# Kernel tuning notes

Measured on AMD Instinct MI355X. Metric: run time of the kernel, lower is better.

The kernel has to match this reference:

```python
import jax, jax.numpy as jnp
import numpy as np

N, D, E = 40000, 128, 640000
ALPHA = 0.1   # GCNII alpha
BETA = 1.0    # GCN2Conv theta=None => beta = 1.0
BN_EPS = 1e-5


def setup_inputs() -> dict:
    key = jax.random.key(0)
    ks = jax.random.split(key, 5)
    x = jax.random.normal(ks[0], (N, D), jnp.float32)
    x_orig = jax.random.normal(ks[1], (N, D), jnp.float32)
    edge_index = jax.random.randint(ks[2], (2, E), 0, N, dtype=jnp.int64)
    edge_weights = jax.random.uniform(ks[3], (E,), jnp.float32)
    W = jax.random.normal(ks[4], (D, D), jnp.float32) / np.sqrt(D).astype(np.float32)
    gamma = jnp.ones((D,), jnp.float32)
    beta = jnp.zeros((D,), jnp.float32)
    return dict(x=x, x_orig=x_orig, edge_index=edge_index,
                edge_weights=edge_weights, W=W, gamma=gamma, beta=beta)


def _gcn_norm(edge_index, edge_weight, num_nodes):
    # PyG gcn_norm: add self loops (weight 1), symmetric D^{-1/2} A D^{-1/2}
    loop = jnp.arange(num_nodes, dtype=edge_index.dtype)
    row = jnp.concatenate([edge_index[0], loop])   # source
    col = jnp.concatenate([edge_index[1], loop])   # target
    ew = jnp.concatenate([edge_weight, jnp.ones((num_nodes,), edge_weight.dtype)])
    deg = jax.ops.segment_sum(ew, col, num_segments=num_nodes)
    dis = jnp.where(deg > 0, jax.lax.rsqrt(deg), 0.0)
    norm = dis[row] * ew * dis[col]
    return row, col, norm


def reference(x, x_orig, edge_index, edge_weights, W, gamma, beta):
    n = x.shape[0]
    row, col, norm = _gcn_norm(edge_index, edge_weights, n)
    # sparse neighbor aggregation: gather x[row], scale, scatter-add to col
    agg = jax.ops.segment_sum(norm[:, None] * x[row], col, num_segments=n)
    # GCNII initial-residual blend; theta=None => out = blended @ W (beta=1)
    h = ((1.0 - ALPHA) * agg + ALPHA * x_orig) @ W
    h = jax.nn.relu(h)
    # BatchNorm1d (training mode: batch statistics, biased variance)
    mean = h.mean(axis=0)
    var = h.var(axis=0)
    h = (h - mean) * jax.lax.rsqrt(var + BN_EPS) * gamma + beta
    return h
```

## Files before the change

### kernel.cpp

```cpp
#include <hip/hip_runtime.h>

#define NN 40000
#define DD 128
#define EE 640000

__global__ __launch_bounds__(256) void k_init(int* __restrict__ cnt,
                                              float* __restrict__ sums) {
    int i = blockIdx.x * 256 + threadIdx.x;
    if (i < NN) cnt[i] = 0;
    if (i < 256) sums[i] = 0.0f;
}

__global__ __launch_bounds__(256) void k_rank(const int* __restrict__ ei,
                                              int* __restrict__ cnt,
                                              int* __restrict__ rank) {
    int e = blockIdx.x * 256 + threadIdx.x;
    int c = ei[EE + e];
    rank[e] = atomicAdd(&cnt[c], 1);
}

#define SCAN_CH 40
__global__ __launch_bounds__(1024) void k_scan(const int* __restrict__ cnt,
                                               int* __restrict__ off) {
    __shared__ int sm[1024];
    int t = threadIdx.x;
    int base = t * SCAN_CH;
    int s = 0;
    if (base < NN) {
#pragma unroll
        for (int i = 0; i < SCAN_CH; ++i) s += cnt[base + i];
    }
    sm[t] = s;
    __syncthreads();
    for (int d = 1; d < 1024; d <<= 1) {
        int v = (t >= d) ? sm[t - d] : 0;
        __syncthreads();
        sm[t] += v;
        __syncthreads();
    }
    if (base < NN) {
        int run = sm[t] - s;
#pragma unroll
        for (int i = 0; i < SCAN_CH; ++i) {
            off[base + i] = run;
            run += cnt[base + i];
        }
    }
    if (t == 1023) off[NN] = sm[1023];
}

__global__ __launch_bounds__(256) void k_permute(const int* __restrict__ ei,
                                                 const float* __restrict__ ew,
                                                 const int* __restrict__ rank,
                                                 const int* __restrict__ off,
                                                 int2* __restrict__ srn) {
    int e = blockIdx.x * 256 + threadIdx.x;
    int r = ei[e], c = ei[EE + e];
    int pos = off[c] + rank[e];
    srn[pos] = make_int2(r, __float_as_int(ew[e]));
}

__global__ __launch_bounds__(256) void k_degdis(const int* __restrict__ off,
                                                const int2* __restrict__ srn,
                                                float* __restrict__ dis) {
    int gid = blockIdx.x * 256 + threadIdx.x;
    int node = gid >> 6;
    int lane = gid & 63;
    int s = off[node], e = off[node + 1];
    float v = 0.0f;
    for (int p = s + lane; p < e; p += 64) v += __int_as_float(srn[p].y);
#pragma unroll
    for (int m = 1; m < 64; m <<= 1) v += __shfl_xor(v, m);
    if (lane == 0) dis[node] = rsqrtf(1.0f + v);
}

__global__ __launch_bounds__(256) void k_gather(const int* __restrict__ off,
                                                const int2* __restrict__ srn,
                                                const float* __restrict__ x,
                                                const float* __restrict__ xorig,
                                                const float* __restrict__ dis,
                                                float* __restrict__ blend) {
    int gid = blockIdx.x * 256 + threadIdx.x;
    int wave = gid >> 6;
    int lane = gid & 63;
    int half = lane >> 5;
    int l32  = lane & 31;
    int node = wave * 2 + half;
    int srcb = half << 5;
    const float4* x4 = (const float4*)x;

    float dc = dis[node];
    float4 sv = x4[(size_t)node * 32 + l32];
    float4 acc0 = {sv.x * dc, sv.y * dc, sv.z * dc, sv.w * dc};
    float4 acc1 = {0, 0, 0, 0}, acc2 = {0, 0, 0, 0}, acc3 = {0, 0, 0, 0};

    int p = off[node], eend = off[node + 1];
    while (__any(p < eend)) {
        int ee = p + l32;
        bool act = ee < eend;
        int2 rv = act ? srn[ee] : make_int2(0, 0);
        float dl = act ? dis[rv.x] : 0.0f;
        float nm = __int_as_float(rv.y) * dl;
        int nb = eend - p;
        nb = nb < 0 ? 0 : (nb > 32 ? 32 : nb);
        int j = 0;
        for (; j + 4 <= nb; j += 4) {
            int r0 = __shfl(rv.x, srcb + j);
            int r1 = __shfl(rv.x, srcb + j + 1);
            int r2 = __shfl(rv.x, srcb + j + 2);
            int r3 = __shfl(rv.x, srcb + j + 3);
            float n0 = __shfl(nm, srcb + j);
            float n1 = __shfl(nm, srcb + j + 1);
            float n2 = __shfl(nm, srcb + j + 2);
            float n3 = __shfl(nm, srcb + j + 3);
            float4 v0 = x4[(size_t)r0 * 32 + l32];
            float4 v1 = x4[(size_t)r1 * 32 + l32];
            float4 v2 = x4[(size_t)r2 * 32 + l32];
            float4 v3 = x4[(size_t)r3 * 32 + l32];
            acc0.x = fmaf(n0, v0.x, acc0.x); acc0.y = fmaf(n0, v0.y, acc0.y);
            acc0.z = fmaf(n0, v0.z, acc0.z); acc0.w = fmaf(n0, v0.w, acc0.w);
            acc1.x = fmaf(n1, v1.x, acc1.x); acc1.y = fmaf(n1, v1.y, acc1.y);
            acc1.z = fmaf(n1, v1.z, acc1.z); acc1.w = fmaf(n1, v1.w, acc1.w);
            acc2.x = fmaf(n2, v2.x, acc2.x); acc2.y = fmaf(n2, v2.y, acc2.y);
            acc2.z = fmaf(n2, v2.z, acc2.z); acc2.w = fmaf(n2, v2.w, acc2.w);
            acc3.x = fmaf(n3, v3.x, acc3.x); acc3.y = fmaf(n3, v3.y, acc3.y);
            acc3.z = fmaf(n3, v3.z, acc3.z); acc3.w = fmaf(n3, v3.w, acc3.w);
        }
        for (; j < nb; ++j) {
            int rr = __shfl(rv.x, srcb + j);
            float nn = __shfl(nm, srcb + j);
            float4 v = x4[(size_t)rr * 32 + l32];
            acc0.x = fmaf(nn, v.x, acc0.x); acc0.y = fmaf(nn, v.y, acc0.y);
            acc0.z = fmaf(nn, v.z, acc0.z); acc0.w = fmaf(nn, v.w, acc0.w);
        }
        p += 32;
    }
    float4 xo = ((const float4*)xorig)[(size_t)node * 32 + l32];
    float4 bl;
    bl.x = 0.9f * (dc * (acc0.x + acc1.x + acc2.x + acc3.x)) + 0.1f * xo.x;
    bl.y = 0.9f * (dc * (acc0.y + acc1.y + acc2.y + acc3.y)) + 0.1f * xo.y;
    bl.z = 0.9f * (dc * (acc0.z + acc1.z + acc2.z + acc3.z)) + 0.1f * xo.z;
    bl.w = 0.9f * (dc * (acc0.w + acc1.w + acc2.w + acc3.w)) + 0.1f * xo.w;
    ((float4*)blend)[(size_t)node * 32 + l32] = bl;
}

__global__ __launch_bounds__(256) void k_matmul(const float* __restrict__ blend,
                                                const float* __restrict__ W,
                                                float* __restrict__ out) {
    int id = blockIdx.x;
    int rowblk, colhalf;
    if (id >= 624) { rowblk = 312; colhalf = id - 624; }
    else { rowblk = ((id >> 4) << 3) | (id & 7); colhalf = (id >> 3) & 1; }

    __shared__ float Wl[DD * 64];
    int t = threadIdx.x;
    int jb = colhalf << 6;
    {
#pragma unroll
        for (int i = 0; i < 8; ++i) {
            int idx = i * 256 + t;
            int k = idx >> 4, jq = idx & 15;
            *(float4*)&Wl[k * 64 + jq * 4] =
                *(const float4*)&W[(size_t)k * DD + jb + jq * 4];
        }
    }
    __syncthreads();

    int rg = t >> 3;
    int cg = t & 7;
    int row0 = rowblk * 128 + rg * 4;
    bool valid = (row0 + 3) < NN;
    size_t rr = valid ? (size_t)row0 : 0;
    int jc = cg * 8;

    float acc[4][8] = {};
    const float* ap = blend + rr * DD;

    for (int k0 = 0; k0 < DD; k0 += 4) {
        float in[4][4];
#pragma unroll
        for (int r = 0; r < 4; ++r) {
            float4 av = *(const float4*)(ap + r * DD + k0);
            in[r][0] = av.x; in[r][1] = av.y; in[r][2] = av.z; in[r][3] = av.w;
        }
#pragma unroll
        for (int kk = 0; kk < 4; ++kk) {
            float4 w0 = *(const float4*)&Wl[(k0 + kk) * 64 + jc];
            float4 w1 = *(const float4*)&Wl[(k0 + kk) * 64 + jc + 4];
#pragma unroll
            for (int r = 0; r < 4; ++r) {
                float a = in[r][kk];
                acc[r][0] = fmaf(a, w0.x, acc[r][0]);
                acc[r][1] = fmaf(a, w0.y, acc[r][1]);
                acc[r][2] = fmaf(a, w0.z, acc[r][2]);
                acc[r][3] = fmaf(a, w0.w, acc[r][3]);
                acc[r][4] = fmaf(a, w1.x, acc[r][4]);
                acc[r][5] = fmaf(a, w1.y, acc[r][5]);
                acc[r][6] = fmaf(a, w1.z, acc[r][6]);
                acc[r][7] = fmaf(a, w1.w, acc[r][7]);
            }
        }
    }
    if (valid) {
#pragma unroll
        for (int r = 0; r < 4; ++r) {
            float* orow = out + (rr + r) * DD + jb + jc;
            float4 v0 = {fmaxf(acc[r][0], 0.0f), fmaxf(acc[r][1], 0.0f),
                         fmaxf(acc[r][2], 0.0f), fmaxf(acc[r][3], 0.0f)};
            float4 v1 = {fmaxf(acc[r][4], 0.0f), fmaxf(acc[r][5], 0.0f),
                         fmaxf(acc[r][6], 0.0f), fmaxf(acc[r][7], 0.0f)};
            *(float4*)(orow) = v0;
            *(float4*)(orow + 4) = v1;
        }
    }
}

__global__ __launch_bounds__(256) void k_stats(const float* __restrict__ h,
                                               float* __restrict__ sums) {
    int t = threadIdx.x;
    int tid = blockIdx.x * 256 + t;
    int cg = t & 31;
    int row0 = tid >> 5;
    float4 s = {0, 0, 0, 0}, q = {0, 0, 0, 0};
    for (int r = row0; r < NN; r += 2048) {
        float4 v = *(const float4*)&h[(size_t)r * DD + cg * 4];
        s.x += v.x; s.y += v.y; s.z += v.z; s.w += v.w;
        q.x += v.x * v.x; q.y += v.y * v.y; q.z += v.z * v.z; q.w += v.w * v.w;
    }
    __shared__ float red[256][8];
    red[t][0] = s.x; red[t][1] = s.y; red[t][2] = s.z; red[t][3] = s.w;
    red[t][4] = q.x; red[t][5] = q.y; red[t][6] = q.z; red[t][7] = q.w;
    __syncthreads();
    if (t < 32) {
#pragma unroll
        for (int s8 = 1; s8 < 8; ++s8)
#pragma unroll
            for (int c = 0; c < 8; ++c) red[t][c] += red[t + 32 * s8][c];
        int j = t * 4;
        unsafeAtomicAdd(&sums[j + 0], red[t][0]);
        unsafeAtomicAdd(&sums[j + 1], red[t][1]);
        unsafeAtomicAdd(&sums[j + 2], red[t][2]);
        unsafeAtomicAdd(&sums[j + 3], red[t][3]);
        unsafeAtomicAdd(&sums[DD + j + 0], red[t][4]);
        unsafeAtomicAdd(&sums[DD + j + 1], red[t][5]);
        unsafeAtomicAdd(&sums[DD + j + 2], red[t][6]);
        unsafeAtomicAdd(&sums[DD + j + 3], red[t][7]);
    }
}

__global__ __launch_bounds__(256) void k_apply(float* __restrict__ h,
                                               const float* __restrict__ sums,
                                               const float* __restrict__ gamma,
                                               const float* __restrict__ beta) {
    int g = blockIdx.x * 256 + threadIdx.x;
    int i = g >> 5, q = g & 31;
    int j = q * 4;
    const float invN = 1.0f / (float)NN;
    float4 sm = *(const float4*)&sums[j];
    float4 sq = *(const float4*)&sums[DD + j];
    float4 gm = *(const float4*)&gamma[j];
    float4 bt = *(const float4*)&beta[j];
    float4 v = *(float4*)&h[(size_t)i * DD + j];
    float m0 = sm.x * invN, m1 = sm.y * invN, m2 = sm.z * invN, m3 = sm.w * invN;
    float i0 = rsqrtf(fmaxf(sq.x * invN - m0 * m0, 0.0f) + 1e-5f);
    float i1 = rsqrtf(fmaxf(sq.y * invN - m1 * m1, 0.0f) + 1e-5f);
    float i2 = rsqrtf(fmaxf(sq.z * invN - m2 * m2, 0.0f) + 1e-5f);
    float i3 = rsqrtf(fmaxf(sq.w * invN - m3 * m3, 0.0f) + 1e-5f);
    v.x = (v.x - m0) * i0 * gm.x + bt.x;
    v.y = (v.y - m1) * i1 * gm.y + bt.y;
    v.z = (v.z - m2) * i2 * gm.z + bt.z;
    v.w = (v.w - m3) * i3 * gm.w + bt.w;
    *(float4*)&h[(size_t)i * DD + j] = v;
}

extern "C" void kernel_launch(void* const* d_in, const int* in_sizes, int n_in,
                              void* d_out, int out_size, void* d_ws, size_t ws_size,
                              hipStream_t stream) {
    const float* x     = (const float*)d_in[0];
    const float* xorig = (const float*)d_in[1];
    const int*   ei    = (const int*)d_in[2];
    const float* ew    = (const float*)d_in[3];
    const float* W     = (const float*)d_in[4];
    const float* gamma = (const float*)d_in[5];
    const float* beta  = (const float*)d_in[6];
    float* out = (float*)d_out;

    float* ws    = (float*)d_ws;
    float* blend = ws;
    int2*  srn   = (int2*)(blend + (size_t)NN * DD);
    float* dis   = (float*)(srn + EE);
    float* sums  = dis + NN;
    int*   cnt   = (int*)(sums + 256);
    int*   off   = cnt + NN;
    int*   rank  = off + NN + 1;

    k_init   <<<160,   256, 0, stream>>>(cnt, sums);
    k_rank   <<<2500,  256, 0, stream>>>(ei, cnt, rank);
    k_scan   <<<1,    1024, 0, stream>>>(cnt, off);
    k_permute<<<2500,  256, 0, stream>>>(ei, ew, rank, off, srn);
    k_degdis <<<10000, 256, 0, stream>>>(off, srn, dis);
    k_gather <<<5000,  256, 0, stream>>>(off, srn, x, xorig, dis, blend);
    k_matmul <<<626,   256, 0, stream>>>(blend, W, out);
    k_stats  <<<256,   256, 0, stream>>>(out, sums);
    k_apply  <<<5000,  256, 0, stream>>>(out, sums, gamma, beta);
}
```

Before: 257.9 us.

## Fuse batchnorm statistics into matmul epilogue and unroll gather by eight

Each matmul block now accumulates per-column sum and sum-of-squares of its ReLU outputs, reduces them in shared memory and atomically adds them into the global sums. This removes the separate stats kernel and its full re-read of the output. The gather loop also now issues eight neighbour row loads per iteration instead of four, to keep more memory requests in flight. The costs are a larger shared-memory footprint in the matmul, more register pressure in the gather, and more atomics (626 blocks instead of 256).

```diff
diff --git a/kernel.cpp b/kernel.cpp
--- a/kernel.cpp
+++ b/kernel.cpp
@@ -91,8 +91,8 @@
 
     float dc = dis[node];
     float4 sv = x4[(size_t)node * 32 + l32];
-    float4 acc0 = {sv.x * dc, sv.y * dc, sv.z * dc, sv.w * dc};
-    float4 acc1 = {0, 0, 0, 0}, acc2 = {0, 0, 0, 0}, acc3 = {0, 0, 0, 0};
+    float4 a0 = {sv.x * dc, sv.y * dc, sv.z * dc, sv.w * dc};
+    float4 a1 = {0, 0, 0, 0}, a2 = {0, 0, 0, 0}, a3 = {0, 0, 0, 0};
 
     int p = off[node], eend = off[node + 1];
     while (__any(p < eend)) {
@@ -104,55 +104,55 @@
         int nb = eend - p;
         nb = nb < 0 ? 0 : (nb > 32 ? 32 : nb);
         int j = 0;
-        for (; j + 4 <= nb; j += 4) {
-            int r0 = __shfl(rv.x, srcb + j);
-            int r1 = __shfl(rv.x, srcb + j + 1);
-            int r2 = __shfl(rv.x, srcb + j + 2);
-            int r3 = __shfl(rv.x, srcb + j + 3);
-            float n0 = __shfl(nm, srcb + j);
-            float n1 = __shfl(nm, srcb + j + 1);
-            float n2 = __shfl(nm, srcb + j + 2);
-            float n3 = __shfl(nm, srcb + j + 3);
-            float4 v0 = x4[(size_t)r0 * 32 + l32];
-            float4 v1 = x4[(size_t)r1 * 32 + l32];
-            float4 v2 = x4[(size_t)r2 * 32 + l32];
-            float4 v3 = x4[(size_t)r3 * 32 + l32];
-            acc0.x = fmaf(n0, v0.x, acc0.x); acc0.y = fmaf(n0, v0.y, acc0.y);
-            acc0.z = fmaf(n0, v0.z, acc0.z); acc0.w = fmaf(n0, v0.w, acc0.w);
-            acc1.x = fmaf(n1, v1.x, acc1.x); acc1.y = fmaf(n1, v1.y, acc1.y);
-            acc1.z = fmaf(n1, v1.z, acc1.z); acc1.w = fmaf(n1, v1.w, acc1.w);
-            acc2.x = fmaf(n2, v2.x, acc2.x); acc2.y = fmaf(n2, v2.y, acc2.y);
-            acc2.z = fmaf(n2, v2.z, acc2.z); acc2.w = fmaf(n2, v2.w, acc2.w);
-            acc3.x = fmaf(n3, v3.x, acc3.x); acc3.y = fmaf(n3, v3.y, acc3.y);
-            acc3.z = fmaf(n3, v3.z, acc3.z); acc3.w = fmaf(n3, v3.w, acc3.w);
+        for (; j + 8 <= nb; j += 8) {
+            int r[8]; float n[8];
+#pragma unroll
+            for (int u = 0; u < 8; ++u) {
+                r[u] = __shfl(rv.x, srcb + j + u);
+                n[u] = __shfl(nm, srcb + j + u);
+            }
+            float4 v[8];
+#pragma unroll
+            for (int u = 0; u < 8; ++u) v[u] = x4[(size_t)r[u] * 32 + l32];
+#pragma unroll
+            for (int u = 0; u < 8; ++u) {
+                float4* ac = (u & 3) == 0 ? &a0 : (u & 3) == 1 ? &a1
+                           : (u & 3) == 2 ? &a2 : &a3;
+                ac->x = fmaf(n[u], v[u].x, ac->x);
+                ac->y = fmaf(n[u], v[u].y, ac->y);
+                ac->z = fmaf(n[u], v[u].z, ac->z);
+                ac->w = fmaf(n[u], v[u].w, ac->w);
+            }
         }
         for (; j < nb; ++j) {
             int rr = __shfl(rv.x, srcb + j);
             float nn = __shfl(nm, srcb + j);
             float4 v = x4[(size_t)rr * 32 + l32];
-            acc0.x = fmaf(nn, v.x, acc0.x); acc0.y = fmaf(nn, v.y, acc0.y);
-            acc0.z = fmaf(nn, v.z, acc0.z); acc0.w = fmaf(nn, v.w, acc0.w);
+            a0.x = fmaf(nn, v.x, a0.x); a0.y = fmaf(nn, v.y, a0.y);
+            a0.z = fmaf(nn, v.z, a0.z); a0.w = fmaf(nn, v.w, a0.w);
         }
         p += 32;
     }
     float4 xo = ((const float4*)xorig)[(size_t)node * 32 + l32];
     float4 bl;
-    bl.x = 0.9f * (dc * (acc0.x + acc1.x + acc2.x + acc3.x)) + 0.1f * xo.x;
-    bl.y = 0.9f * (dc * (acc0.y + acc1.y + acc2.y + acc3.y)) + 0.1f * xo.y;
-    bl.z = 0.9f * (dc * (acc0.z + acc1.z + acc2.z + acc3.z)) + 0.1f * xo.z;
-    bl.w = 0.9f * (dc * (acc0.w + acc1.w + acc2.w + acc3.w)) + 0.1f * xo.w;
+    bl.x = 0.9f * (dc * (a0.x + a1.x + a2.x + a3.x)) + 0.1f * xo.x;
+    bl.y = 0.9f * (dc * (a0.y + a1.y + a2.y + a3.y)) + 0.1f * xo.y;
+    bl.z = 0.9f * (dc * (a0.z + a1.z + a2.z + a3.z)) + 0.1f * xo.z;
+    bl.w = 0.9f * (dc * (a0.w + a1.w + a2.w + a3.w)) + 0.1f * xo.w;
     ((float4*)blend)[(size_t)node * 32 + l32] = bl;
 }
 
 __global__ __launch_bounds__(256) void k_matmul(const float* __restrict__ blend,
                                                 const float* __restrict__ W,
-                                                float* __restrict__ out) {
+                                                float* __restrict__ out,
+                                                float* __restrict__ sums) {
     int id = blockIdx.x;
     int rowblk, colhalf;
     if (id >= 624) { rowblk = 312; colhalf = id - 624; }
     else { rowblk = ((id >> 4) << 3) | (id & 7); colhalf = (id >> 3) & 1; }
 
     __shared__ float Wl[DD * 64];
+    __shared__ float red[256][16];
     int t = threadIdx.x;
     int jb = colhalf << 6;
     {
@@ -201,50 +201,35 @@
             }
         }
     }
+    float ls[8] = {}, lq[8] = {};
     if (valid) {
 #pragma unroll
         for (int r = 0; r < 4; ++r) {
+#pragma unroll
+            for (int c = 0; c < 8; ++c) {
+                float v = fmaxf(acc[r][c], 0.0f);
+                acc[r][c] = v;
+                ls[c] += v;
+                lq[c] += v * v;
+            }
             float* orow = out + (rr + r) * DD + jb + jc;
-            float4 v0 = {fmaxf(acc[r][0], 0.0f), fmaxf(acc[r][1], 0.0f),
-                         fmaxf(acc[r][2], 0.0f), fmaxf(acc[r][3], 0.0f)};
-            float4 v1 = {fmaxf(acc[r][4], 0.0f), fmaxf(acc[r][5], 0.0f),
-                         fmaxf(acc[r][6], 0.0f), fmaxf(acc[r][7], 0.0f)};
-            *(float4*)(orow) = v0;
-            *(float4*)(orow + 4) = v1;
-        }
-    }
-}
-
-__global__ __launch_bounds__(256) void k_stats(const float* __restrict__ h,
-                                               float* __restrict__ sums) {
-    int t = threadIdx.x;
-    int tid = blockIdx.x * 256 + t;
-    int cg = t & 31;
-    int row0 = tid >> 5;
-    float4 s = {0, 0, 0, 0}, q = {0, 0, 0, 0};
-    for (int r = row0; r < NN; r += 2048) {
-        float4 v = *(const float4*)&h[(size_t)r * DD + cg * 4];
-        s.x += v.x; s.y += v.y; s.z += v.z; s.w += v.w;
-        q.x += v.x * v.x; q.y += v.y * v.y; q.z += v.z * v.z; q.w += v.w * v.w;
-    }
-    __shared__ float red[256][8];
-    red[t][0] = s.x; red[t][1] = s.y; red[t][2] = s.z; red[t][3] = s.w;
-    red[t][4] = q.x; red[t][5] = q.y; red[t][6] = q.z; red[t][7] = q.w;
+            *(float4*)(orow)     = *(float4*)&acc[r][0];
+            *(float4*)(orow + 4) = *(float4*)&acc[r][4];
+        }
+    }
+#pragma unroll
+    for (int c = 0; c < 8; ++c) { red[t][c] = ls[c]; red[t][8 + c] = lq[c]; }
     __syncthreads();
-    if (t < 32) {
-#pragma unroll
-        for (int s8 = 1; s8 < 8; ++s8)
-#pragma unroll
-            for (int c = 0; c < 8; ++c) red[t][c] += red[t + 32 * s8][c];
-        int j = t * 4;
-        unsafeAtomicAdd(&sums[j + 0], red[t][0]);
-        unsafeAtomicAdd(&sums[j + 1], red[t][1]);
-        unsafeAtomicAdd(&sums[j + 2], red[t][2]);
-        unsafeAtomicAdd(&sums[j + 3], red[t][3]);
-        unsafeAtomicAdd(&sums[DD + j + 0], red[t][4]);
-        unsafeAtomicAdd(&sums[DD + j + 1], red[t][5]);
-        unsafeAtomicAdd(&sums[DD + j + 2], red[t][6]);
-        unsafeAtomicAdd(&sums[DD + j + 3], red[t][7]);
+    if (t < 64) {
+        int cg2 = t >> 3, c2 = t & 7;
+        float s = 0.f, q = 0.f;
+#pragma unroll
+        for (int rg2 = 0; rg2 < 32; ++rg2) {
+            s += red[rg2 * 8 + cg2][c2];
+            q += red[rg2 * 8 + cg2][8 + c2];
+        }
+        unsafeAtomicAdd(&sums[jb + cg2 * 8 + c2], s);
+        unsafeAtomicAdd(&sums[DD + jb + cg2 * 8 + c2], q);
     }
 }
 
@@ -300,7 +285,6 @@
     k_permute<<<2500,  256, 0, stream>>>(ei, ew, rank, off, srn);
     k_degdis <<<10000, 256, 0, stream>>>(off, srn, dis);
     k_gather <<<5000,  256, 0, stream>>>(off, srn, x, xorig, dis, blend);
-    k_matmul <<<626,   256, 0, stream>>>(blend, W, out);
-    k_stats  <<<256,   256, 0, stream>>>(out, sums);
+    k_matmul <<<626,   256, 0, stream>>>(blend, W, out, sums);
     k_apply  <<<5000,  256, 0, stream>>>(out, sums, gamma, beta);
 }
```

Measured after the change: 230.2 us. 1.12x faster.
